# Kernel optimization log

Hardware: AMD Instinct MI355X
Metric: run time of the kernel (lower is better)

The kernel has to match this reference:

```python
import jax, jax.numpy as jnp
import numpy as np

D = 1024       # in_features == out_features
H = 4096       # hidden_features
E = 8          # num_experts
K = 2          # top_k


def setup_inputs() -> dict:
    key = jax.random.key(0)
    ks = jax.random.split(key, 7)
    x = jax.random.normal(ks[0], (2, 2048, D), dtype=jnp.float32)
    # router linear (torch Linear: y = x @ W.T + b, W is [out, in])
    Wr = jax.random.normal(ks[1], (E, D), dtype=jnp.float32) * 0.02
    br = jnp.zeros((E,), dtype=jnp.float32)
    # per-expert MLP params stacked on leading expert axis
    W1 = jax.random.normal(ks[2], (E, H, D), dtype=jnp.float32) * 0.02
    b1 = jnp.zeros((E, H), dtype=jnp.float32)
    W2 = jax.random.normal(ks[3], (E, D, H), dtype=jnp.float32) * 0.02
    b2 = jnp.zeros((E, D), dtype=jnp.float32)
    return {"x": x, "Wr": Wr, "br": br, "W1": W1, "b1": b1, "W2": W2, "b2": b2}


def reference(x, Wr, br, W1, b1, W2, b2):
    B, S, Din = x.shape
    x_flat = x.reshape(-1, Din)                       # [T, D]
    # --- router: softmax then top-k gates ---
    logits = x_flat @ Wr.T + br                       # [T, E]
    gates = jax.nn.softmax(logits, axis=-1)
    top_g, top_i = jax.lax.top_k(gates, K)            # [T, K]
    # per-(token, expert) combine weight; topk indices are distinct so sum == select
    w = jnp.sum(jax.nn.one_hot(top_i, E, dtype=gates.dtype) * top_g[..., None], axis=1)  # [T, E]
    # --- experts (dropout p=0.0 is identity; torch GELU default is exact erf) ---
    h = jax.nn.gelu(jnp.einsum('td,ehd->eth', x_flat, W1) + b1[:, None, :], approximate=False)  # [E, T, H]
    y = jnp.einsum('eth,edh->etd', h, W2) + b2[:, None, :]                                       # [E, T, D]
    # --- combine: weighted sum over experts (zero weight for unrouted pairs) ---
    out = jnp.einsum('te,etd->td', w, y)              # [T, D]
    return out.reshape(B, S, Din)
```

## Files before the change

### kernel.cpp

```cpp
#include <hip/hip_runtime.h>
#include <hip/hip_bf16.h>

#define Dd 1024
#define Hh 4096
#define Ee 8
#define Tt 4096
#define Kk 2

typedef __attribute__((ext_vector_type(8))) short short8;
typedef __attribute__((ext_vector_type(4))) float f32x4;

__device__ __forceinline__ unsigned short f2bf_bits(float f) {
  unsigned u = __builtin_bit_cast(unsigned, f);
  u += 0x7FFFu + ((u >> 16) & 1u);
  return (unsigned short)(u >> 16);
}

__device__ __forceinline__ unsigned pack2bf(float lo, float hi) {
  return (unsigned)f2bf_bits(lo) | ((unsigned)f2bf_bits(hi) << 16);
}

__device__ __forceinline__ float fast_gelu(float v) {
  float z = v * 0.70710678118654752f;
  float az = fabsf(z);
  float t = __frcp_rn(1.0f + 0.3275911f * az);
  float poly = t * (0.254829592f + t * (-0.284496736f + t * (1.421413741f +
               t * (-1.453152027f + t * 1.061405429f))));
  float e = __expf(-az * az);
  float erf_az = 1.0f - poly * e;
  float erf_z = copysignf(erf_az, z);
  return 0.5f * v * (1.0f + erf_z);
}

__device__ __forceinline__ void glds16(const void* g, void* l) {
  __builtin_amdgcn_global_load_lds(
      (const __attribute__((address_space(1))) unsigned int*)g,
      (__attribute__((address_space(3))) unsigned int*)l, 16, 0, 0);
}

__global__ __launch_bounds__(256) void cvt_router_kernel(
    const float* __restrict__ x, const float* __restrict__ Wr, const float* __restrict__ br,
    const float* __restrict__ w1, unsigned short* __restrict__ w1b,
    int* __restrict__ tokinfo, float* __restrict__ g2) {
  const int RB = Tt / 4;
  if (blockIdx.x < RB) {
    int t = blockIdx.x * 4 + (threadIdx.x >> 6);
    int lane = threadIdx.x & 63;
    const float4* x4 = reinterpret_cast<const float4*>(x + (size_t)t * Dd);
    const float4* Wr4 = reinterpret_cast<const float4*>(Wr);
    float pe[Ee];
#pragma unroll
    for (int e = 0; e < Ee; e++) pe[e] = 0.f;
    for (int c = lane; c < Dd / 4; c += 64) {
      float4 xv = x4[c];
#pragma unroll
      for (int e = 0; e < Ee; e++) {
        float4 wv = Wr4[e * (Dd / 4) + c];
        pe[e] += xv.x * wv.x + xv.y * wv.y + xv.z * wv.z + xv.w * wv.w;
      }
    }
#pragma unroll
    for (int e = 0; e < Ee; e++) {
      float v = pe[e];
#pragma unroll
      for (int s = 32; s > 0; s >>= 1) v += __shfl_xor(v, s);
      pe[e] = v + br[e];
    }
    if (lane == 0) {
      float mx = pe[0];
#pragma unroll
      for (int e = 1; e < Ee; e++) mx = fmaxf(mx, pe[e]);
      float g[Ee];
      float sum = 0.f;
#pragma unroll
      for (int e = 0; e < Ee; e++) { g[e] = expf(pe[e] - mx); sum += g[e]; }
      float inv = 1.0f / sum;
      int e0 = 0; float g0v = g[0];
#pragma unroll
      for (int e = 1; e < Ee; e++) if (g[e] > g0v) { g0v = g[e]; e0 = e; }
      int e1 = -1; float g1v = -1.f;
#pragma unroll
      for (int e = 0; e < Ee; e++) if (e != e0 && g[e] > g1v) { g1v = g[e]; e1 = e; }
      g2[t * 2 + 0] = g0v * inv;
      g2[t * 2 + 1] = g1v * inv;
      tokinfo[t] = e0 | (e1 << 8);
    }
  } else {
    const int n8 = Ee * Hh * Dd / 8;
    int i = (blockIdx.x - RB) * 256 + threadIdx.x;
    int stride = (gridDim.x - RB) * 256;
    const float4* src = reinterpret_cast<const float4*>(w1);
    uint4* dst = reinterpret_cast<uint4*>(w1b);
    for (; i < n8; i += stride) {
      float4 a = src[2 * i], b = src[2 * i + 1];
      uint4 o;
      o.x = pack2bf(a.x, a.y);
      o.y = pack2bf(a.z, a.w);
      o.z = pack2bf(b.x, b.y);
      o.w = pack2bf(b.z, b.w);
      dst[i] = o;
    }
  }
}

__global__ void assign_kernel(const int* __restrict__ tokinfo, int* __restrict__ pos,
                              int* __restrict__ list, int* __restrict__ cnt) {
  __shared__ int lc[Ee];
  int tid = threadIdx.x;
  if (tid < Ee) lc[tid] = 0;
  __syncthreads();
  for (int t = tid; t < Tt; t += 256) {
    int info = tokinfo[t];
    int e0 = info & 255, e1 = info >> 8;
    int p0 = atomicAdd(&lc[e0], 1);
    list[e0 * Tt + p0] = t * 2;
    pos[t * 2] = (e0 << 16) | p0;
    int p1 = atomicAdd(&lc[e1], 1);
    list[e1 * Tt + p1] = t * 2 + 1;
    pos[t * 2 + 1] = (e1 << 16) | p1;
  }
  __syncthreads();
  if (tid < Ee) cnt[tid] = lc[tid];
}

__global__ __launch_bounds__(256) void gather_kernel(
    const float* __restrict__ x, const int* __restrict__ pos,
    unsigned short* __restrict__ xg) {
  int t = blockIdx.x * 4 + (threadIdx.x >> 6);
  int lane = threadIdx.x & 63;
  int pk0 = pos[t * 2], pk1 = pos[t * 2 + 1];
  uint4* r0 = (uint4*)(xg + ((size_t)(pk0 >> 16) * Tt + (pk0 & 0xffff)) * Dd);
  uint4* r1 = (uint4*)(xg + ((size_t)(pk1 >> 16) * Tt + (pk1 & 0xffff)) * Dd);
  const float4* x4 = reinterpret_cast<const float4*>(x + (size_t)t * Dd);
#pragma unroll
  for (int it = 0; it < 2; ++it) {
    int c = lane + it * 64;
    float4 a = x4[2 * c], b = x4[2 * c + 1];
    uint4 o;
    o.x = pack2bf(a.x, a.y);
    o.y = pack2bf(a.z, a.w);
    o.z = pack2bf(b.x, b.y);
    o.w = pack2bf(b.z, b.w);
    r0[c] = o;
    r1[c] = o;
  }
}

#define STAGE(so_, k0)                                 \
  do {                                                 \
    glds16(aS0 + (k0), AsW + (so_) * 4096);            \
    glds16(aS1 + (k0), AsW + (so_) * 4096 + 2048);     \
    glds16(bS0 + (k0), BsW + (so_) * 4096);            \
    glds16(bS1 + (k0), BsW + (so_) * 4096 + 2048);     \
  } while (0)

#define COMPUTE(so_)                                                            \
  do {                                                                          \
    short8 af[4], bv[4];                                                        \
    _Pragma("unroll") for (int i = 0; i < 4; i++)                               \
        af[i] = *reinterpret_cast<const short8*>(                               \
            &As[(so_) * 4096 + (wm * 64 + i * 16 + fr) * 32 + gph]);            \
    _Pragma("unroll") for (int j = 0; j < 4; j++)                               \
        bv[j] = *reinterpret_cast<const short8*>(                               \
            &Bs[(so_) * 4096 + (wn * 64 + j * 16 + fr) * 32 + gph]);            \
    _Pragma("unroll") for (int i = 0; i < 4; i++)                               \
      _Pragma("unroll") for (int j = 0; j < 4; j++)                             \
          acc[i][j] = __builtin_amdgcn_mfma_f32_16x16x32_bf16(af[i], bv[j],     \
                                                              acc[i][j], 0, 0, 0); \
  } while (0)

#define PIPELINE(NKT)                                              \
  do {                                                             \
    STAGE(0, 0);                                                   \
    STAGE(1, 32);                                                  \
    for (int kt = 0; kt <= (NKT)-3; ++kt) {                        \
      int so = kt & 1;                                             \
      asm volatile("s_waitcnt vmcnt(4)" ::: "memory");             \
      __builtin_amdgcn_s_barrier();                                \
      COMPUTE(so);                                                 \
      __builtin_amdgcn_s_barrier();                                \
      STAGE(so, (kt + 2) * 32);                                    \
    }                                                              \
    asm volatile("s_waitcnt vmcnt(4)" ::: "memory");               \
    __builtin_amdgcn_s_barrier();                                  \
    COMPUTE(((NKT)-2) & 1);                                        \
    asm volatile("s_waitcnt vmcnt(0)" ::: "memory");               \
    __builtin_amdgcn_s_barrier();                                  \
    COMPUTE(((NKT)-1) & 1);                                        \
  } while (0)

#define EXPERT_META                                    \
  int ce = cnt[e];                                     \
  int off_e = 0;                                       \
  _Pragma("unroll") for (int i_ = 0; i_ < Ee; i_++)    \
      off_e += (i_ < e) ? cnt[i_] : 0;                 \
  int m_e = (ce + 127) >> 7;

__global__ __launch_bounds__(256) void gemm1_cvtw2_kernel(
    const unsigned short* __restrict__ xg, const unsigned short* __restrict__ w1b,
    const float* __restrict__ b1,
    const int* __restrict__ cnt,
    unsigned short* __restrict__ hb,
    const float* __restrict__ w2, unsigned short* __restrict__ w2b) {
  const int GB = 2048;
  __shared__ short As[2 * 4096];
  __shared__ short Bs[2 * 4096];

  if (blockIdx.x >= GB) {
    const int n8 = Ee * Dd * Hh / 8;
    int i = (blockIdx.x - GB) * 256 + threadIdx.x;
    int stride = (gridDim.x - GB) * 256;
    const float4* src = reinterpret_cast<const float4*>(w2);
    uint4* dst = reinterpret_cast<uint4*>(w2b);
    for (; i < n8; i += stride) {
      float4 a = src[2 * i], b = src[2 * i + 1];
      uint4 o;
      o.x = pack2bf(a.x, a.y);
      o.y = pack2bf(a.z, a.w);
      o.z = pack2bf(b.x, b.y);
      o.w = pack2bf(b.z, b.w);
      dst[i] = o;
    }
    return;
  }

  int e = blockIdx.x & 7;
  const int G = GB >> 3;
  EXPERT_META
  int span = m_e * (Hh / 128);

  int tid = threadIdx.x;
  int lane = tid & 63;
  int w = tid >> 6;
  int wm = w >> 1, wn = w & 1;
  int fr = lane & 15, kq = lane >> 4;

  int r0 = tid >> 2;
  int swz = ((tid & 3) ^ ((r0 >> 1) & 3)) << 3;
  short* AsW = &As[w * 512];
  short* BsW = &Bs[w * 512];
  int gph = (kq ^ ((fr >> 1) & 3)) << 3;
  const float* b1e = b1 + (size_t)e * Hh;

  for (int local = blockIdx.x >> 3; local < span; local += G) {
    int nt = local / m_e, mt = local % m_e;
    __syncthreads();

    const unsigned short* aS0 = xg + (size_t)e * Tt * Dd + (size_t)(mt * 128 + r0) * Dd + swz;
    const unsigned short* aS1 = aS0 + (size_t)64 * Dd;
    const unsigned short* bS0 = w1b + (size_t)e * Hh * Dd + (size_t)(nt * 128 + r0) * Dd + swz;
    const unsigned short* bS1 = bS0 + (size_t)64 * Dd;

    float biasj[4];
#pragma unroll
    for (int j = 0; j < 4; j++) biasj[j] = b1e[nt * 128 + wn * 64 + j * 16 + fr];
    asm volatile("s_waitcnt vmcnt(0)" ::: "memory");

    f32x4 acc[4][4] = {};
    PIPELINE(Dd / 32);

#pragma unroll
    for (int i = 0; i < 4; i++) {
      int rb = wm * 64 + i * 16 + kq * 4;
#pragma unroll
      for (int j = 0; j < 4; j++) {
        int col = nt * 128 + wn * 64 + j * 16 + fr;
#pragma unroll
        for (int rr = 0; rr < 4; rr++) {
          int grow = mt * 128 + rb + rr;
          if (grow < ce) {
            float v = fast_gelu(acc[i][j][rr] + biasj[j]);
            hb[(size_t)(off_e + grow) * Hh + col] = f2bf_bits(v);
          }
        }
      }
    }
  }
}

__global__ __launch_bounds__(256) void gemm2_kernel(
    const unsigned short* __restrict__ hb, const unsigned short* __restrict__ w2b,
    const float* __restrict__ b2,
    const int* __restrict__ cnt, const int* __restrict__ list,
    float* __restrict__ y) {
  int e = blockIdx.x & 7;
  int G = gridDim.x >> 3;
  EXPERT_META
  int span = m_e * (Dd / 128);

  __shared__ short As[2 * 4096];
  __shared__ short Bs[2 * 4096];

  int tid = threadIdx.x;
  int lane = tid & 63;
  int w = tid >> 6;
  int wm = w >> 1, wn = w & 1;
  int fr = lane & 15, kq = lane >> 4;

  int r0 = tid >> 2;
  int swz = ((tid & 3) ^ ((r0 >> 1) & 3)) << 3;
  short* AsW = &As[w * 512];
  short* BsW = &Bs[w * 512];
  int gph = (kq ^ ((fr >> 1) & 3)) << 3;
  const int* le = list + e * Tt;
  const float* b2e = b2 + (size_t)e * Dd;

  for (int local = blockIdx.x >> 3; local < span; local += G) {
    int nt = local / m_e, mt = local % m_e;
    __syncthreads();

    int ra0 = mt * 128 + r0;      if (ra0 >= ce) ra0 = ce - 1;
    int ra1 = mt * 128 + r0 + 64; if (ra1 >= ce) ra1 = ce - 1;
    const unsigned short* aS0 = hb + (size_t)(off_e + ra0) * Hh + swz;
    const unsigned short* aS1 = hb + (size_t)(off_e + ra1) * Hh + swz;
    const unsigned short* bS0 = w2b + (size_t)e * Dd * Hh + (size_t)(nt * 128 + r0) * Hh + swz;
    const unsigned short* bS1 = bS0 + (size_t)64 * Hh;

    float biasj[4];
#pragma unroll
    for (int j = 0; j < 4; j++) biasj[j] = b2e[nt * 128 + wn * 64 + j * 16 + fr];
    asm volatile("s_waitcnt vmcnt(0)" ::: "memory");

    f32x4 acc[4][4] = {};
    PIPELINE(Hh / 32);

#pragma unroll
    for (int i = 0; i < 4; i++) {
      int rb = wm * 64 + i * 16 + kq * 4;
#pragma unroll
      for (int j = 0; j < 4; j++) {
        int col = nt * 128 + wn * 64 + j * 16 + fr;
#pragma unroll
        for (int rr = 0; rr < 4; rr++) {
          int grow = mt * 128 + rb + rr;
          if (grow < ce) {
            int en = le[grow];
            y[(size_t)en * Dd + col] = acc[i][j][rr] + biasj[j];
          }
        }
      }
    }
  }
}

__global__ __launch_bounds__(256) void combine_kernel(
    const float* __restrict__ y, const float* __restrict__ g2, float* __restrict__ out) {
  const int C4 = Dd / 4;
  int i = blockIdx.x * blockDim.x + threadIdx.x;
  int t = i / C4;
  int c = i % C4;
  float g0 = g2[t * 2 + 0];
  float g1 = g2[t * 2 + 1];
  float4 y0 = reinterpret_cast<const float4*>(y)[(size_t)(t * 2 + 0) * C4 + c];
  float4 y1 = reinterpret_cast<const float4*>(y)[(size_t)(t * 2 + 1) * C4 + c];
  float4 o;
  o.x = g0 * y0.x + g1 * y1.x;
  o.y = g0 * y0.y + g1 * y1.y;
  o.z = g0 * y0.z + g1 * y1.z;
  o.w = g0 * y0.w + g1 * y1.w;
  reinterpret_cast<float4*>(out)[i] = o;
}

extern "C" void kernel_launch(void* const* d_in, const int* in_sizes, int n_in,
                              void* d_out, int out_size, void* d_ws, size_t ws_size,
                              hipStream_t stream) {
  const float* x  = (const float*)d_in[0];
  const float* Wr = (const float*)d_in[1];
  const float* br = (const float*)d_in[2];
  const float* W1 = (const float*)d_in[3];
  const float* b1 = (const float*)d_in[4];
  const float* W2 = (const float*)d_in[5];
  const float* b2 = (const float*)d_in[6];
  float* out = (float*)d_out;

  char* base = (char*)d_ws;
  size_t o = 0;
  auto alloc = [&](size_t n) { char* r = base + o; o += (n + 255) & ~(size_t)255; return r; };
  unsigned short* w1b = (unsigned short*)alloc((size_t)Ee * Hh * Dd * 2);
  unsigned short* w2b = (unsigned short*)alloc((size_t)Ee * Dd * Hh * 2);
  unsigned short* xg  = (unsigned short*)alloc((size_t)Ee * Tt * Dd * 2);
  unsigned short* hb  = (unsigned short*)alloc((size_t)(Tt * Kk + 256) * Hh * 2);
  int* list  = (int*)alloc((size_t)Ee * Tt * 4);
  float* g2  = (float*)alloc((size_t)Tt * Kk * 4);
  int* tokinfo = (int*)alloc(Tt * 4);
  int* pos   = (int*)alloc((size_t)Tt * Kk * 4);
  int* cnt   = (int*)alloc(Ee * 4);
  if (o > ws_size) return;

  float* y = (float*)w1b;

  cvt_router_kernel<<<1024 + 4096, 256, 0, stream>>>(x, Wr, br, W1, w1b, tokinfo, g2);
  assign_kernel<<<1, 256, 0, stream>>>(tokinfo, pos, list, cnt);
  gather_kernel<<<Tt / 4, 256, 0, stream>>>(x, pos, xg);

  gemm1_cvtw2_kernel<<<2048 + 4096, 256, 0, stream>>>(xg, w1b, b1, cnt, hb, W2, w2b);
  gemm2_kernel<<<1024, 256, 0, stream>>>(hb, w2b, b2, cnt, list, y);
  combine_kernel<<<(Tt * Dd / 4) / 256, 256, 0, stream>>>(y, g2, out);
}
```

Before: 371.9 us.

## Fuse token gather into GEMM1 loads via routing list, drop gather kernel

The router kernel now also writes a dense bf16 copy of x. The separate gather kernel and pos array are removed. GEMM1 instead reads A rows indirectly through the per-expert token list, clamping out-of-range rows to the last valid one. This cuts one kernel launch and the doubled gathered-activation write, at the cost of non-contiguous A-row loads inside GEMM1. The GEMM2 grid is also halved.

```diff
diff --git a/kernel.cpp b/kernel.cpp
--- a/kernel.cpp
+++ b/kernel.cpp
@@ -41,7 +41,8 @@
 __global__ __launch_bounds__(256) void cvt_router_kernel(
     const float* __restrict__ x, const float* __restrict__ Wr, const float* __restrict__ br,
     const float* __restrict__ w1, unsigned short* __restrict__ w1b,
-    int* __restrict__ tokinfo, float* __restrict__ g2) {
+    int* __restrict__ tokinfo, float* __restrict__ g2,
+    unsigned short* __restrict__ xb) {
   const int RB = Tt / 4;
   if (blockIdx.x < RB) {
     int t = blockIdx.x * 4 + (threadIdx.x >> 6);
@@ -58,6 +59,18 @@
         float4 wv = Wr4[e * (Dd / 4) + c];
         pe[e] += xv.x * wv.x + xv.y * wv.y + xv.z * wv.z + xv.w * wv.w;
       }
+    }
+    uint4* xbr = (uint4*)(xb + (size_t)t * Dd);
+#pragma unroll
+    for (int it = 0; it < 2; ++it) {
+      int c = lane + it * 64;
+      float4 a = x4[2 * c], b = x4[2 * c + 1];
+      uint4 o;
+      o.x = pack2bf(a.x, a.y);
+      o.y = pack2bf(a.z, a.w);
+      o.z = pack2bf(b.x, b.y);
+      o.w = pack2bf(b.z, b.w);
+      xbr[c] = o;
     }
 #pragma unroll
     for (int e = 0; e < Ee; e++) {
@@ -103,7 +116,7 @@
   }
 }
 
-__global__ void assign_kernel(const int* __restrict__ tokinfo, int* __restrict__ pos,
+__global__ void assign_kernel(const int* __restrict__ tokinfo,
                               int* __restrict__ list, int* __restrict__ cnt) {
   __shared__ int lc[Ee];
   int tid = threadIdx.x;
@@ -114,36 +127,11 @@
     int e0 = info & 255, e1 = info >> 8;
     int p0 = atomicAdd(&lc[e0], 1);
     list[e0 * Tt + p0] = t * 2;
-    pos[t * 2] = (e0 << 16) | p0;
     int p1 = atomicAdd(&lc[e1], 1);
     list[e1 * Tt + p1] = t * 2 + 1;
-    pos[t * 2 + 1] = (e1 << 16) | p1;
   }
   __syncthreads();
   if (tid < Ee) cnt[tid] = lc[tid];
-}
-
-__global__ __launch_bounds__(256) void gather_kernel(
-    const float* __restrict__ x, const int* __restrict__ pos,
-    unsigned short* __restrict__ xg) {
-  int t = blockIdx.x * 4 + (threadIdx.x >> 6);
-  int lane = threadIdx.x & 63;
-  int pk0 = pos[t * 2], pk1 = pos[t * 2 + 1];
-  uint4* r0 = (uint4*)(xg + ((size_t)(pk0 >> 16) * Tt + (pk0 & 0xffff)) * Dd);
-  uint4* r1 = (uint4*)(xg + ((size_t)(pk1 >> 16) * Tt + (pk1 & 0xffff)) * Dd);
-  const float4* x4 = reinterpret_cast<const float4*>(x + (size_t)t * Dd);
-#pragma unroll
-  for (int it = 0; it < 2; ++it) {
-    int c = lane + it * 64;
-    float4 a = x4[2 * c], b = x4[2 * c + 1];
-    uint4 o;
-    o.x = pack2bf(a.x, a.y);
-    o.y = pack2bf(a.z, a.w);
-    o.z = pack2bf(b.x, b.y);
-    o.w = pack2bf(b.z, b.w);
-    r0[c] = o;
-    r1[c] = o;
-  }
 }
 
 #define STAGE(so_, k0)                                 \
@@ -197,9 +185,9 @@
   int m_e = (ce + 127) >> 7;
 
 __global__ __launch_bounds__(256) void gemm1_cvtw2_kernel(
-    const unsigned short* __restrict__ xg, const unsigned short* __restrict__ w1b,
+    const unsigned short* __restrict__ xb, const unsigned short* __restrict__ w1b,
     const float* __restrict__ b1,
-    const int* __restrict__ cnt,
+    const int* __restrict__ cnt, const int* __restrict__ list,
     unsigned short* __restrict__ hb,
     const float* __restrict__ w2, unsigned short* __restrict__ w2b) {
   const int GB = 2048;
@@ -241,13 +229,18 @@
   short* BsW = &Bs[w * 512];
   int gph = (kq ^ ((fr >> 1) & 3)) << 3;
   const float* b1e = b1 + (size_t)e * Hh;
+  const int* le = list + e * Tt;
 
   for (int local = blockIdx.x >> 3; local < span; local += G) {
     int nt = local / m_e, mt = local % m_e;
     __syncthreads();
 
-    const unsigned short* aS0 = xg + (size_t)e * Tt * Dd + (size_t)(mt * 128 + r0) * Dd + swz;
-    const unsigned short* aS1 = aS0 + (size_t)64 * Dd;
+    int ga0 = mt * 128 + r0;      if (ga0 >= ce) ga0 = ce - 1;
+    int ga1 = mt * 128 + r0 + 64; if (ga1 >= ce) ga1 = ce - 1;
+    int tok0 = le[ga0] >> 1;
+    int tok1 = le[ga1] >> 1;
+    const unsigned short* aS0 = xb + (size_t)tok0 * Dd + swz;
+    const unsigned short* aS1 = xb + (size_t)tok1 * Dd + swz;
     const unsigned short* bS0 = w1b + (size_t)e * Hh * Dd + (size_t)(nt * 128 + r0) * Dd + swz;
     const unsigned short* bS1 = bS0 + (size_t)64 * Dd;
 
@@ -378,22 +371,20 @@
   auto alloc = [&](size_t n) { char* r = base + o; o += (n + 255) & ~(size_t)255; return r; };
   unsigned short* w1b = (unsigned short*)alloc((size_t)Ee * Hh * Dd * 2);
   unsigned short* w2b = (unsigned short*)alloc((size_t)Ee * Dd * Hh * 2);
-  unsigned short* xg  = (unsigned short*)alloc((size_t)Ee * Tt * Dd * 2);
+  unsigned short* xb  = (unsigned short*)alloc((size_t)Tt * Dd * 2);
   unsigned short* hb  = (unsigned short*)alloc((size_t)(Tt * Kk + 256) * Hh * 2);
   int* list  = (int*)alloc((size_t)Ee * Tt * 4);
   float* g2  = (float*)alloc((size_t)Tt * Kk * 4);
   int* tokinfo = (int*)alloc(Tt * 4);
-  int* pos   = (int*)alloc((size_t)Tt * Kk * 4);
   int* cnt   = (int*)alloc(Ee * 4);
   if (o > ws_size) return;
 
   float* y = (float*)w1b;
 
-  cvt_router_kernel<<<1024 + 4096, 256, 0, stream>>>(x, Wr, br, W1, w1b, tokinfo, g2);
-  assign_kernel<<<1, 256, 0, stream>>>(tokinfo, pos, list, cnt);
-  gather_kernel<<<Tt / 4, 256, 0, stream>>>(x, pos, xg);
-
-  gemm1_cvtw2_kernel<<<2048 + 4096, 256, 0, stream>>>(xg, w1b, b1, cnt, hb, W2, w2b);
-  gemm2_kernel<<<1024, 256, 0, stream>>>(hb, w2b, b2, cnt, list, y);
+  cvt_router_kernel<<<1024 + 4096, 256, 0, stream>>>(x, Wr, br, W1, w1b, tokinfo, g2, xb);
+  assign_kernel<<<1, 256, 0, stream>>>(tokinfo, list, cnt);
+
+  gemm1_cvtw2_kernel<<<2048 + 4096, 256, 0, stream>>>(xb, w1b, b1, cnt, list, hb, W2, w2b);
+  gemm2_kernel<<<512, 256, 0, stream>>>(hb, w2b, b2, cnt, list, y);
   combine_kernel<<<(Tt * Dd / 4) / 256, 256, 0, stream>>>(y, g2, out);
 }
```

Result: faster. 357.7 us (median of 2 runs) (-3.8%).
